# Optimization experiments

Measured on AMD Instinct MI355X. Metric: run time of the kernel, lower is better.

The kernel has to match this reference:

```python
import jax, jax.numpy as jnp
import numpy as np

B, H, W_DIM, C = 16, 128, 128, 256

def setup_inputs() -> dict:
    key = jax.random.key(0)
    k1, k2, k3 = jax.random.split(key, 3)
    grid = jax.random.normal(k1, (B, H, W_DIM, C), dtype=jnp.float32)
    # nn.Linear(2C, C): weight [C, 2C], bias [C]; store transposed for x @ W
    W = jax.random.normal(k2, (2 * C, C), dtype=jnp.float32) * (1.0 / np.sqrt(2 * C))
    b = jax.random.normal(k3, (C,), dtype=jnp.float32) * 0.01
    return {"grid": grid, "W": W, "b": b}

def reference(grid, W, b):
    # cumulative max along width (axis=2) and height (axis=1)
    x_cummax = jax.lax.cummax(grid, axis=2)
    y_cummax = jax.lax.cummax(grid, axis=1)
    result = jnp.concatenate([x_cummax, y_cummax], axis=-1)  # [B,H,W,2C]
    return result @ W + b  # [B,H,W,C]
```

## Files before the change

kernel.cpp:

```cpp
#include <hip/hip_runtime.h>
#include <hip/hip_fp16.h>

#define BB 16
#define HH 128
#define WW 128
#define CC 256

typedef __attribute__((ext_vector_type(8))) short s16x8;
typedef __attribute__((ext_vector_type(8))) unsigned short u16x8;
typedef __attribute__((ext_vector_type(4))) float f32x4;
typedef __attribute__((ext_vector_type(4))) int i32x4;

__device__ static inline unsigned short f2bf(float x) {
    union { float f; unsigned u; } v; v.f = x;
    unsigned r = v.u + 0x7fffu + ((v.u >> 16) & 1u);
    return (unsigned short)(r >> 16);
}
__device__ static inline float bf2f(unsigned short u) {
    union { unsigned u; float f; } v; v.u = (unsigned)u << 16; return v.f;
}
__device__ static inline unsigned short h2u(__half h) {
    unsigned short u; __builtin_memcpy(&u, &h, 2); return u;
}
__device__ static inline float u2f16(unsigned short u) {
    __half h; __builtin_memcpy(&h, &u, 2); return __half2float(h);
}
__device__ static inline int sidx(int row, int col) {
    return row * 256 + (((col >> 3) ^ (row & 7)) << 3) + (col & 7);
}
__device__ static inline int sidx4(int row, int c4) {
    return row * 256 + (((c4 >> 1) ^ (row & 7)) << 3) + (c4 & 1) * 4;
}

__global__ __launch_bounds__(256) void conv_w_kernel(const float* __restrict__ Wf,
                                                     unsigned short* __restrict__ Wt) {
    const int i = blockIdx.x * 256 + threadIdx.x;
    const int n = i & 255, k = i >> 8;
    const int hy = k >> 8, g = (k >> 3) & 31, j = k & 7;
    Wt[hy * 65536 + ((size_t)(g * 256 + n) << 3) + j] = f2bf(Wf[i]);
}

__device__ __forceinline__ void scan16_to_lds(const float4* __restrict__ base, size_t st,
                                              unsigned short* __restrict__ As,
                                              unsigned short* __restrict__ smax,
                                              int c4, int s) {
    const int row0 = s * 16;
    float4 buf[8], nxt[8];
    #pragma unroll
    for (int j = 0; j < 8; ++j) buf[j] = base[(size_t)j * st];
    __builtin_amdgcn_sched_group_barrier(0x20, 8, 0);
    #pragma unroll
    for (int j = 0; j < 8; ++j) nxt[j] = base[(size_t)(8 + j) * st];
    __builtin_amdgcn_sched_group_barrier(0x20, 8, 0);
    float4 run = make_float4(-3.4e38f, -3.4e38f, -3.4e38f, -3.4e38f);
    #pragma unroll
    for (int j = 0; j < 8; ++j) {
        run.x = fmaxf(run.x, buf[j].x); run.y = fmaxf(run.y, buf[j].y);
        run.z = fmaxf(run.z, buf[j].z); run.w = fmaxf(run.w, buf[j].w);
        ushort4 o; o.x = f2bf(run.x); o.y = f2bf(run.y); o.z = f2bf(run.z); o.w = f2bf(run.w);
        *(ushort4*)(As + sidx4(row0 + j, c4)) = o;
    }
    #pragma unroll
    for (int j = 0; j < 8; ++j) {
        run.x = fmaxf(run.x, nxt[j].x); run.y = fmaxf(run.y, nxt[j].y);
        run.z = fmaxf(run.z, nxt[j].z); run.w = fmaxf(run.w, nxt[j].w);
        ushort4 o; o.x = f2bf(run.x); o.y = f2bf(run.y); o.z = f2bf(run.z); o.w = f2bf(run.w);
        *(ushort4*)(As + sidx4(row0 + 8 + j, c4)) = o;
    }
    ushort4 sm; sm.x = f2bf(run.x); sm.y = f2bf(run.y); sm.z = f2bf(run.z); sm.w = f2bf(run.w);
    *(ushort4*)(smax + s * 256 + c4 * 4) = sm;
}

__device__ __forceinline__ void carry_apply(unsigned short* __restrict__ As,
                                            const unsigned short* __restrict__ smax,
                                            int c4, int s) {
    if (s == 0) return;
    float4 cf = make_float4(-3.4e38f, -3.4e38f, -3.4e38f, -3.4e38f);
    for (int k = 0; k < s; ++k) {
        const ushort4 m = *(const ushort4*)(smax + k * 256 + c4 * 4);
        cf.x = fmaxf(cf.x, bf2f(m.x)); cf.y = fmaxf(cf.y, bf2f(m.y));
        cf.z = fmaxf(cf.z, bf2f(m.z)); cf.w = fmaxf(cf.w, bf2f(m.w));
    }
    ushort4 cb; cb.x = f2bf(cf.x); cb.y = f2bf(cf.y); cb.z = f2bf(cf.z); cb.w = f2bf(cf.w);
    const int row0 = s * 16;
    #pragma unroll
    for (int r = 0; r < 16; ++r) {
        unsigned short* pp = As + sidx4(row0 + r, c4);
        ushort4 v = *(ushort4*)(pp);
        ushort4 o;
        o.x = (bf2f(v.x) >= cf.x) ? v.x : cb.x;
        o.y = (bf2f(v.y) >= cf.y) ? v.y : cb.y;
        o.z = (bf2f(v.z) >= cf.z) ? v.z : cb.z;
        o.w = (bf2f(v.w) >= cf.w) ? v.w : cb.w;
        *(ushort4*)(pp) = o;
    }
}

__device__ __forceinline__ void gemm_stage(unsigned short* __restrict__ As,
                                           const s16x8* __restrict__ Wv, int t) {
    const int lane = t & 63, wid = t >> 6;
    const int wr = wid >> 2, wn = wid & 3;
    f32x4 acc[4][4];
    #pragma unroll
    for (int i = 0; i < 4; ++i)
        #pragma unroll
        for (int j = 0; j < 4; ++j) acc[i][j] = (f32x4){0.f, 0.f, 0.f, 0.f};

    #pragma unroll
    for (int q = 0; q < 8; ++q) {
        const int g = q * 4 + (lane >> 4);
        s16x8 af[4], bf[4];
        #pragma unroll
        for (int fm = 0; fm < 4; ++fm) {
            const int row = wr * 64 + fm * 16 + (lane & 15);
            af[fm] = *(const s16x8*)(As + row * 256 + ((g ^ (row & 7)) << 3));
        }
        #pragma unroll
        for (int fn = 0; fn < 4; ++fn)
            bf[fn] = Wv[g * 256 + wn * 64 + fn * 16 + (lane & 15)];
        #pragma unroll
        for (int fm = 0; fm < 4; ++fm)
            #pragma unroll
            for (int fn = 0; fn < 4; ++fn)
                acc[fm][fn] = __builtin_amdgcn_mfma_f32_16x16x32_bf16(
                    af[fm], bf[fn], acc[fm][fn], 0, 0, 0);
    }
    __syncthreads();
    #pragma unroll
    for (int fn = 0; fn < 4; ++fn) {
        const int col = wn * 64 + fn * 16 + (lane & 15);
        #pragma unroll
        for (int fm = 0; fm < 4; ++fm) {
            const int rbase = wr * 64 + fm * 16 + ((lane >> 4) << 2);
            #pragma unroll
            for (int r = 0; r < 4; ++r)
                As[sidx(rbase + r, col)] = h2u(__float2half(acc[fm][fn][r]));
        }
    }
    __syncthreads();
}

__global__ __launch_bounds__(512, 4) void hscan_gemm_kernel(const float* __restrict__ grid,
                                                            const unsigned short* __restrict__ Wt,
                                                            unsigned short* __restrict__ partial) {
    __shared__ unsigned short As[32768];
    __shared__ unsigned short smax[2048];
    const int t = threadIdx.x;
    const int c4 = t & 63, s = t >> 6;
    const int b = blockIdx.x >> 7;
    const int w = blockIdx.x & 127;

    const float4* base = (const float4*)(grid + ((size_t)(b * 128 + s * 16) * 128 + w) * 256) + c4;
    scan16_to_lds(base, 8192, As, smax, c4, s);
    __syncthreads();
    carry_apply(As, smax, c4, s);
    __syncthreads();

    gemm_stage(As, (const s16x8*)(Wt + 65536), t);

    #pragma unroll
    for (int it = 0; it < 8; ++it) {
        const int f = it * 4096 + t * 8;
        const int row = f >> 8, col = f & 255;
        const i32x4 v = *(const i32x4*)(As + sidx(row, col));
        *(i32x4*)(partial + (((size_t)b * 128 + row) * 128 + w) * 256 + col) = v;
    }
}

__global__ __launch_bounds__(512, 4) void wscan_gemm_kernel(const float* __restrict__ grid,
                                                            const unsigned short* __restrict__ Wt,
                                                            const unsigned short* __restrict__ partial,
                                                            const float* __restrict__ bias,
                                                            float* __restrict__ out) {
    __shared__ unsigned short As[32768];
    __shared__ unsigned short smax[2048];
    const int t = threadIdx.x;
    const int c4 = t & 63, s = t >> 6;
    const size_t bh = blockIdx.x;

    const float4* base = (const float4*)(grid + (bh * 128 + (size_t)(s * 16)) * 256) + c4;
    scan16_to_lds(base, 64, As, smax, c4, s);
    __syncthreads();
    carry_apply(As, smax, c4, s);
    __syncthreads();

    gemm_stage(As, (const s16x8*)Wt, t);

    const int colf = (t * 8) & 255;
    float bv[8];
    #pragma unroll
    for (int k = 0; k < 8; ++k) bv[k] = bias[colf + k];

    #pragma unroll
    for (int it = 0; it < 8; ++it) {
        const int f = it * 4096 + t * 8;
        const int row = f >> 8, col = f & 255;
        const u16x8 lv = *(const u16x8*)(As + sidx(row, col));
        const size_t gi = (bh * 128 + row) * 256 + col;
        const u16x8 pv = *(const u16x8*)(partial + gi);
        f32x4 o0, o1;
        #pragma unroll
        for (int k = 0; k < 4; ++k)
            o0[k] = u2f16((unsigned short)lv[k]) + u2f16((unsigned short)pv[k]) + bv[k];
        #pragma unroll
        for (int k = 0; k < 4; ++k)
            o1[k] = u2f16((unsigned short)lv[4 + k]) + u2f16((unsigned short)pv[4 + k]) + bv[4 + k];
        *(f32x4*)(out + gi)     = o0;
        *(f32x4*)(out + gi + 4) = o1;
    }
}

extern "C" void kernel_launch(void* const* d_in, const int* in_sizes, int n_in,
                              void* d_out, int out_size, void* d_ws, size_t ws_size,
                              hipStream_t stream) {
    const float* grid = (const float*)d_in[0];
    const float* Wf   = (const float*)d_in[1];
    const float* bias = (const float*)d_in[2];
    float* out        = (float*)d_out;

    unsigned short* partial = (unsigned short*)d_ws;
    unsigned short* Wt      = (unsigned short*)((char*)d_ws + (size_t)134217728);

    conv_w_kernel<<<512, 256, 0, stream>>>(Wf, Wt);
    hscan_gemm_kernel<<<2048, 512, 0, stream>>>(grid, Wt, partial);
    wscan_gemm_kernel<<<2048, 512, 0, stream>>>(grid, Wt, partial, bias, out);
}
```

Before: 257.8 us.

## Split each scan line into two 64-row halves with prefix-max carry recompute

Each block now handles half of a 128-long scan line (64 rows) instead of the full line. The second-half block rereads and reduces the first half from global memory to get the carry max. Halving LDS per block and the GEMM tile allows more blocks per CU (launch bounds raised from 4 to 6) and doubles the grid. Block indices are also remapped so adjacent lines share an XCD, for better L2 locality. The cost is extra global reads of the first half for half the blocks.

```diff
diff --git a/kernel.cpp b/kernel.cpp
--- a/kernel.cpp
+++ b/kernel.cpp
@@ -30,6 +30,10 @@
 }
 __device__ static inline int sidx4(int row, int c4) {
     return row * 256 + (((c4 >> 1) ^ (row & 7)) << 3) + (c4 & 1) * 4;
+}
+__device__ static inline ushort4 pack4(float4 v) {
+    ushort4 o; o.x = f2bf(v.x); o.y = f2bf(v.y); o.z = f2bf(v.z); o.w = f2bf(v.w);
+    return o;
 }
 
 __global__ __launch_bounds__(256) void conv_w_kernel(const float* __restrict__ Wf,
@@ -40,86 +44,97 @@
     Wt[hy * 65536 + ((size_t)(g * 256 + n) << 3) + j] = f2bf(Wf[i]);
 }
 
-__device__ __forceinline__ void scan16_to_lds(const float4* __restrict__ base, size_t st,
-                                              unsigned short* __restrict__ As,
-                                              unsigned short* __restrict__ smax,
-                                              int c4, int s) {
-    const int row0 = s * 16;
-    float4 buf[8], nxt[8];
-    #pragma unroll
-    for (int j = 0; j < 8; ++j) buf[j] = base[(size_t)j * st];
+__device__ __forceinline__ void scan64(const float4* __restrict__ gbase,
+                                       const float4* __restrict__ pbase,
+                                       size_t st, int hf,
+                                       unsigned short* __restrict__ As,
+                                       unsigned short* __restrict__ smax,
+                                       unsigned short* __restrict__ pmax,
+                                       int c4, int s) {
+    float4 buf[8];
+    #pragma unroll
+    for (int j = 0; j < 8; ++j) buf[j] = gbase[(size_t)j * st];
     __builtin_amdgcn_sched_group_barrier(0x20, 8, 0);
-    #pragma unroll
-    for (int j = 0; j < 8; ++j) nxt[j] = base[(size_t)(8 + j) * st];
-    __builtin_amdgcn_sched_group_barrier(0x20, 8, 0);
+    float4 pbuf[8];
+    if (hf) {
+        #pragma unroll
+        for (int j = 0; j < 8; ++j) pbuf[j] = pbase[(size_t)j * st];
+        __builtin_amdgcn_sched_group_barrier(0x20, 8, 0);
+    }
+    const int row0 = s * 8;
     float4 run = make_float4(-3.4e38f, -3.4e38f, -3.4e38f, -3.4e38f);
     #pragma unroll
     for (int j = 0; j < 8; ++j) {
         run.x = fmaxf(run.x, buf[j].x); run.y = fmaxf(run.y, buf[j].y);
         run.z = fmaxf(run.z, buf[j].z); run.w = fmaxf(run.w, buf[j].w);
-        ushort4 o; o.x = f2bf(run.x); o.y = f2bf(run.y); o.z = f2bf(run.z); o.w = f2bf(run.w);
-        *(ushort4*)(As + sidx4(row0 + j, c4)) = o;
-    }
-    #pragma unroll
-    for (int j = 0; j < 8; ++j) {
-        run.x = fmaxf(run.x, nxt[j].x); run.y = fmaxf(run.y, nxt[j].y);
-        run.z = fmaxf(run.z, nxt[j].z); run.w = fmaxf(run.w, nxt[j].w);
-        ushort4 o; o.x = f2bf(run.x); o.y = f2bf(run.y); o.z = f2bf(run.z); o.w = f2bf(run.w);
-        *(ushort4*)(As + sidx4(row0 + 8 + j, c4)) = o;
-    }
-    ushort4 sm; sm.x = f2bf(run.x); sm.y = f2bf(run.y); sm.z = f2bf(run.z); sm.w = f2bf(run.w);
-    *(ushort4*)(smax + s * 256 + c4 * 4) = sm;
-}
-
-__device__ __forceinline__ void carry_apply(unsigned short* __restrict__ As,
-                                            const unsigned short* __restrict__ smax,
-                                            int c4, int s) {
-    if (s == 0) return;
+        *(ushort4*)(As + sidx4(row0 + j, c4)) = pack4(run);
+    }
+    *(ushort4*)(smax + s * 256 + c4 * 4) = pack4(run);
+    if (hf) {
+        float4 pm = make_float4(-3.4e38f, -3.4e38f, -3.4e38f, -3.4e38f);
+        #pragma unroll
+        for (int j = 0; j < 8; ++j) {
+            pm.x = fmaxf(pm.x, pbuf[j].x); pm.y = fmaxf(pm.y, pbuf[j].y);
+            pm.z = fmaxf(pm.z, pbuf[j].z); pm.w = fmaxf(pm.w, pbuf[j].w);
+        }
+        *(ushort4*)(pmax + s * 256 + c4 * 4) = pack4(pm);
+    }
+    __syncthreads();
     float4 cf = make_float4(-3.4e38f, -3.4e38f, -3.4e38f, -3.4e38f);
+    if (hf) {
+        #pragma unroll
+        for (int k = 0; k < 8; ++k) {
+            const ushort4 m = *(const ushort4*)(pmax + k * 256 + c4 * 4);
+            cf.x = fmaxf(cf.x, bf2f(m.x)); cf.y = fmaxf(cf.y, bf2f(m.y));
+            cf.z = fmaxf(cf.z, bf2f(m.z)); cf.w = fmaxf(cf.w, bf2f(m.w));
+        }
+    }
     for (int k = 0; k < s; ++k) {
         const ushort4 m = *(const ushort4*)(smax + k * 256 + c4 * 4);
         cf.x = fmaxf(cf.x, bf2f(m.x)); cf.y = fmaxf(cf.y, bf2f(m.y));
         cf.z = fmaxf(cf.z, bf2f(m.z)); cf.w = fmaxf(cf.w, bf2f(m.w));
     }
-    ushort4 cb; cb.x = f2bf(cf.x); cb.y = f2bf(cf.y); cb.z = f2bf(cf.z); cb.w = f2bf(cf.w);
-    const int row0 = s * 16;
-    #pragma unroll
-    for (int r = 0; r < 16; ++r) {
-        unsigned short* pp = As + sidx4(row0 + r, c4);
-        ushort4 v = *(ushort4*)(pp);
-        ushort4 o;
-        o.x = (bf2f(v.x) >= cf.x) ? v.x : cb.x;
-        o.y = (bf2f(v.y) >= cf.y) ? v.y : cb.y;
-        o.z = (bf2f(v.z) >= cf.z) ? v.z : cb.z;
-        o.w = (bf2f(v.w) >= cf.w) ? v.w : cb.w;
-        *(ushort4*)(pp) = o;
-    }
-}
-
-__device__ __forceinline__ void gemm_stage(unsigned short* __restrict__ As,
-                                           const s16x8* __restrict__ Wv, int t) {
+    if (hf || s) {
+        const ushort4 cb = pack4(cf);
+        #pragma unroll
+        for (int r = 0; r < 8; ++r) {
+            unsigned short* pp = As + sidx4(row0 + r, c4);
+            ushort4 v = *(ushort4*)pp;
+            ushort4 o;
+            o.x = (bf2f(v.x) >= cf.x) ? v.x : cb.x;
+            o.y = (bf2f(v.y) >= cf.y) ? v.y : cb.y;
+            o.z = (bf2f(v.z) >= cf.z) ? v.z : cb.z;
+            o.w = (bf2f(v.w) >= cf.w) ? v.w : cb.w;
+            *(ushort4*)pp = o;
+        }
+    }
+    __syncthreads();
+}
+
+__device__ __forceinline__ void gemm_stage64(unsigned short* __restrict__ As,
+                                             const s16x8* __restrict__ Wv, int t) {
     const int lane = t & 63, wid = t >> 6;
-    const int wr = wid >> 2, wn = wid & 3;
-    f32x4 acc[4][4];
-    #pragma unroll
-    for (int i = 0; i < 4; ++i)
+    const int wm = wid >> 2, wn = wid & 3;
+    f32x4 acc[2][4];
+    #pragma unroll
+    for (int i = 0; i < 2; ++i)
         #pragma unroll
         for (int j = 0; j < 4; ++j) acc[i][j] = (f32x4){0.f, 0.f, 0.f, 0.f};
 
     #pragma unroll
     for (int q = 0; q < 8; ++q) {
         const int g = q * 4 + (lane >> 4);
-        s16x8 af[4], bf[4];
-        #pragma unroll
-        for (int fm = 0; fm < 4; ++fm) {
-            const int row = wr * 64 + fm * 16 + (lane & 15);
+        s16x8 af[2], bf[4];
+        #pragma unroll
+        for (int fm = 0; fm < 2; ++fm) {
+            const int row = wm * 32 + fm * 16 + (lane & 15);
             af[fm] = *(const s16x8*)(As + row * 256 + ((g ^ (row & 7)) << 3));
         }
         #pragma unroll
         for (int fn = 0; fn < 4; ++fn)
             bf[fn] = Wv[g * 256 + wn * 64 + fn * 16 + (lane & 15)];
         #pragma unroll
-        for (int fm = 0; fm < 4; ++fm)
+        for (int fm = 0; fm < 2; ++fm)
             #pragma unroll
             for (int fn = 0; fn < 4; ++fn)
                 acc[fm][fn] = __builtin_amdgcn_mfma_f32_16x16x32_bf16(
@@ -130,8 +145,8 @@
     for (int fn = 0; fn < 4; ++fn) {
         const int col = wn * 64 + fn * 16 + (lane & 15);
         #pragma unroll
-        for (int fm = 0; fm < 4; ++fm) {
-            const int rbase = wr * 64 + fm * 16 + ((lane >> 4) << 2);
+        for (int fm = 0; fm < 2; ++fm) {
+            const int rbase = wm * 32 + fm * 16 + ((lane >> 4) << 2);
             #pragma unroll
             for (int r = 0; r < 4; ++r)
                 As[sidx(rbase + r, col)] = h2u(__float2half(acc[fm][fn][r]));
@@ -140,64 +155,75 @@
     __syncthreads();
 }
 
-__global__ __launch_bounds__(512, 4) void hscan_gemm_kernel(const float* __restrict__ grid,
+__global__ __launch_bounds__(512, 6) void hscan_gemm_kernel(const float* __restrict__ grid,
                                                             const unsigned short* __restrict__ Wt,
                                                             unsigned short* __restrict__ partial) {
-    __shared__ unsigned short As[32768];
+    __shared__ unsigned short As[16384];
     __shared__ unsigned short smax[2048];
+    __shared__ unsigned short pmax[2048];
     const int t = threadIdx.x;
     const int c4 = t & 63, s = t >> 6;
-    const int b = blockIdx.x >> 7;
-    const int w = blockIdx.x & 127;
-
-    const float4* base = (const float4*)(grid + ((size_t)(b * 128 + s * 16) * 128 + w) * 256) + c4;
-    scan16_to_lds(base, 8192, As, smax, c4, s);
-    __syncthreads();
-    carry_apply(As, smax, c4, s);
-    __syncthreads();
-
-    gemm_stage(As, (const s16x8*)(Wt + 65536), t);
-
-    #pragma unroll
-    for (int it = 0; it < 8; ++it) {
+    const int bid = blockIdx.x;
+    const int xcd = bid & 7, idx = bid >> 3;
+    const int hf  = idx & 1;
+    const int line = xcd * 256 + (idx >> 1);
+    const int b = line >> 7, w = line & 127;
+
+    const float4* gbase = (const float4*)(grid +
+        (((size_t)(b * 128 + hf * 64 + s * 8)) * 128 + w) * 256) + c4;
+    const float4* pbase = (const float4*)(grid +
+        (((size_t)(b * 128 + s * 8)) * 128 + w) * 256) + c4;
+    scan64(gbase, pbase, 8192, hf, As, smax, pmax, c4, s);
+
+    gemm_stage64(As, (const s16x8*)(Wt + 65536), t);
+
+    unsigned short* pb = partial + ((size_t)line * 128 + hf * 64) * 256;
+    #pragma unroll
+    for (int it = 0; it < 4; ++it) {
         const int f = it * 4096 + t * 8;
         const int row = f >> 8, col = f & 255;
         const i32x4 v = *(const i32x4*)(As + sidx(row, col));
-        *(i32x4*)(partial + (((size_t)b * 128 + row) * 128 + w) * 256 + col) = v;
-    }
-}
-
-__global__ __launch_bounds__(512, 4) void wscan_gemm_kernel(const float* __restrict__ grid,
+        *(i32x4*)(pb + f) = v;
+    }
+}
+
+__global__ __launch_bounds__(512, 6) void wscan_gemm_kernel(const float* __restrict__ grid,
                                                             const unsigned short* __restrict__ Wt,
                                                             const unsigned short* __restrict__ partial,
                                                             const float* __restrict__ bias,
                                                             float* __restrict__ out) {
-    __shared__ unsigned short As[32768];
+    __shared__ unsigned short As[16384];
     __shared__ unsigned short smax[2048];
+    __shared__ unsigned short pmax[2048];
     const int t = threadIdx.x;
     const int c4 = t & 63, s = t >> 6;
-    const size_t bh = blockIdx.x;
-
-    const float4* base = (const float4*)(grid + (bh * 128 + (size_t)(s * 16)) * 256) + c4;
-    scan16_to_lds(base, 64, As, smax, c4, s);
-    __syncthreads();
-    carry_apply(As, smax, c4, s);
-    __syncthreads();
-
-    gemm_stage(As, (const s16x8*)Wt, t);
+    const int bid = blockIdx.x;
+    const int xcd = bid & 7, idx = bid >> 3;
+    const int hf  = idx & 1;
+    const int line = xcd * 256 + (idx >> 1);
+    const int b = line >> 7, h = line & 127;
+
+    const float4* gbase = (const float4*)(grid +
+        ((size_t)line * 128 + hf * 64 + s * 8) * 256) + c4;
+    const float4* pbase = (const float4*)(grid +
+        ((size_t)line * 128 + s * 8) * 256) + c4;
+    scan64(gbase, pbase, 64, hf, As, smax, pmax, c4, s);
+
+    gemm_stage64(As, (const s16x8*)Wt, t);
 
     const int colf = (t * 8) & 255;
     float bv[8];
     #pragma unroll
     for (int k = 0; k < 8; ++k) bv[k] = bias[colf + k];
 
-    #pragma unroll
-    for (int it = 0; it < 8; ++it) {
+    float* ob = out + ((size_t)line * 128 + hf * 64) * 256;
+    #pragma unroll
+    for (int it = 0; it < 4; ++it) {
         const int f = it * 4096 + t * 8;
         const int row = f >> 8, col = f & 255;
         const u16x8 lv = *(const u16x8*)(As + sidx(row, col));
-        const size_t gi = (bh * 128 + row) * 256 + col;
-        const u16x8 pv = *(const u16x8*)(partial + gi);
+        const size_t pi = (((size_t)b * 128 + hf * 64 + row) * 128 + h) * 256 + col;
+        const u16x8 pv = *(const u16x8*)(partial + pi);
         f32x4 o0, o1;
         #pragma unroll
         for (int k = 0; k < 4; ++k)
@@ -205,8 +231,8 @@
         #pragma unroll
         for (int k = 0; k < 4; ++k)
             o1[k] = u2f16((unsigned short)lv[4 + k]) + u2f16((unsigned short)pv[4 + k]) + bv[4 + k];
-        *(f32x4*)(out + gi)     = o0;
-        *(f32x4*)(out + gi + 4) = o1;
+        *(f32x4*)(ob + f)     = o0;
+        *(f32x4*)(ob + f + 4) = o1;
     }
 }
 
@@ -222,6 +248,6 @@
     unsigned short* Wt      = (unsigned short*)((char*)d_ws + (size_t)134217728);
 
     conv_w_kernel<<<512, 256, 0, stream>>>(Wf, Wt);
-    hscan_gemm_kernel<<<2048, 512, 0, stream>>>(grid, Wt, partial);
-    wscan_gemm_kernel<<<2048, 512, 0, stream>>>(grid, Wt, partial, bias, out);
-}
+    hscan_gemm_kernel<<<4096, 512, 0, stream>>>(grid, Wt, partial);
+    wscan_gemm_kernel<<<4096, 512, 0, stream>>>(grid, Wt, partial, bias, out);
+}
```

Result: slower. 316.6 us (+22.8%).
